# Kernel optimization log

Measured on AMD Instinct MI355X. Metric: run time of the kernel, lower is better.

Reference implementation:

```python
import jax, jax.numpy as jnp
import numpy as np

DT = 0.1    # arg.DELTA_T
BOX = 1.0   # arg.WORLD_SIZE
B = 8388608


def range_angle(ang):
    # wrap angle to [-pi, pi)
    return jnp.mod(ang + np.pi, 2.0 * np.pi) - np.pi


def setup_inputs() -> dict:
    key = jax.random.key(0)
    k1, k2, k3, k4, k5, k6 = jax.random.split(key, 6)
    x = jax.random.normal(k1, (B, 5), dtype=jnp.float32)          # [px,py,ang,vel,ang_vel]
    a = jax.random.uniform(k2, (B, 2), dtype=jnp.float32)          # actions [a_v, a_w]
    noise = jax.random.normal(k3, (B, 2), dtype=jnp.float32)       # standard-normal process noise
    pro_gains = jax.random.uniform(k4, (2,), dtype=jnp.float32)    # process gains
    pro_noise_ln_vars = jax.random.normal(k5, (2,), dtype=jnp.float32)  # log-variances
    goal_radius = jax.random.uniform(k6, (1,), dtype=jnp.float32)
    return {"x": x, "a": a, "noise": noise, "pro_gains": pro_gains,
            "pro_noise_ln_vars": pro_noise_ln_vars, "goal_radius": goal_radius}


def reference(x, a, noise, pro_gains, pro_noise_ln_vars, goal_radius):
    px, py, ang = x[:, 0], x[:, 1], x[:, 2]
    # w = sqrt(exp(ln_var)) * randn(2)  (noise pre-sampled, deterministic)
    std = jnp.sqrt(jnp.exp(pro_noise_ln_vars))            # [2]
    w = std * noise                                        # [B,2]
    vel = pro_gains[0] * a[:, 0] + w[:, 0]                 # 0*vel drops old vel
    ang_vel = pro_gains[1] * a[:, 1] + w[:, 1]
    ang = range_angle(ang + ang_vel * DT)
    px = jnp.clip(px + vel * jnp.cos(ang) * DT, -BOX, BOX)
    py = jnp.clip(py + vel * jnp.sin(ang) * DT, -BOX, BOX)
    next_x = jnp.stack([px, py, ang, vel, ang_vel], axis=-1)   # [B,5]
    reached_target = jnp.sqrt(px * px + py * py) <= goal_radius[0]  # [B] bool
    return next_x, reached_target
```

## Files before the change

kernel.cpp:

```cpp
#include <hip/hip_runtime.h>
#include <math.h>


__device__ __forceinline__ void step_one(
    float px0, float py0, float ang0,
    float ax, float ay, float n0, float n1,
    float g0, float g1, float std0, float std1, float gr,
    float& px, float& py, float& ang, float& vel, float& ang_vel, float& reach)
{
    const float DT    = 0.1f;
    const float PI_F  = 3.14159265358979323846f;
    const float TWOPI = 6.283185307179586f;

    const float w0 = __fmul_rn(std0, n0);
    const float w1 = __fmul_rn(std1, n1);
    vel     = __fadd_rn(__fmul_rn(g0, ax), w0);
    ang_vel = __fadd_rn(__fmul_rn(g1, ay), w1);

    const float t  = __fadd_rn(ang0, __fmul_rn(ang_vel, DT));
    const float tp = __fadd_rn(t, PI_F);
    float m = fmodf(tp, TWOPI);
    if (m < 0.0f) m = __fadd_rn(m, TWOPI);
    ang = __fsub_rn(m, PI_F);

    float s, c;
    sincosf(ang, &s, &c);

    px = __fadd_rn(px0, __fmul_rn(__fmul_rn(vel, c), DT));
    px = fminf(fmaxf(px, -1.0f), 1.0f);
    py = __fadd_rn(py0, __fmul_rn(__fmul_rn(vel, s), DT));
    py = fminf(fmaxf(py, -1.0f), 1.0f);

    const float r2 = __fadd_rn(__fmul_rn(px, px), __fmul_rn(py, py));
    const float r  = __fsqrt_rn(r2);
    reach = (r <= gr) ? 1.0f : 0.0f;
}

__global__ __launch_bounds__(256) void step_kernel(
    const float* __restrict__ x,
    const float* __restrict__ a,
    const float* __restrict__ noise,
    const float* __restrict__ pro_gains,
    const float* __restrict__ pro_noise_ln_vars,
    const float* __restrict__ goal_radius,
    float* __restrict__ out_next,
    float* __restrict__ out_reach,
    int n)
{
    const int nq = n >> 2;
    const int t = blockIdx.x * blockDim.x + threadIdx.x;

    const float g0   = pro_gains[0];
    const float g1   = pro_gains[1];
    const float std0 = __fsqrt_rn(expf(pro_noise_ln_vars[0]));
    const float std1 = __fsqrt_rn(expf(pro_noise_ln_vars[1]));
    const float gr   = goal_radius[0];

    if (t < nq) {
        const size_t st = (size_t)t;

        const float4* __restrict__ xq = (const float4*)x;
        const float4 q0 = xq[5 * st + 0];
        const float4 q1 = xq[5 * st + 1];
        const float4 q2 = xq[5 * st + 2];
        const float4 q3 = xq[5 * st + 3];
        const float4 q4 = xq[5 * st + 4];

        const float4* __restrict__ aq = (const float4*)a;
        const float4 av0 = aq[2 * st + 0];
        const float4 av1 = aq[2 * st + 1];
        const float4* __restrict__ nqv = (const float4*)noise;
        const float4 nv0 = nqv[2 * st + 0];
        const float4 nv1 = nqv[2 * st + 1];

        const float ipx[4]  = { q0.x, q1.y, q2.z, q3.w };
        const float ipy[4]  = { q0.y, q1.z, q2.w, q4.x };
        const float iang[4] = { q0.z, q1.w, q3.x, q4.y };
        const float iax[4]  = { av0.x, av0.z, av1.x, av1.z };
        const float iay[4]  = { av0.y, av0.w, av1.y, av1.w };
        const float in0[4]  = { nv0.x, nv0.z, nv1.x, nv1.z };
        const float in1[4]  = { nv0.y, nv0.w, nv1.y, nv1.w };

        float opx[4], opy[4], oang[4], ovel[4], oavl[4], orch[4];
#pragma unroll
        for (int k = 0; k < 4; ++k) {
            step_one(ipx[k], ipy[k], iang[k], iax[k], iay[k], in0[k], in1[k],
                     g0, g1, std0, std1, gr,
                     opx[k], opy[k], oang[k], ovel[k], oavl[k], orch[k]);
        }

        float4* __restrict__ oq = (float4*)out_next;
        oq[5 * st + 0] = make_float4(opx[0], opy[0], oang[0], ovel[0]);
        oq[5 * st + 1] = make_float4(oavl[0], opx[1], opy[1], oang[1]);
        oq[5 * st + 2] = make_float4(ovel[1], oavl[1], opx[2], opy[2]);
        oq[5 * st + 3] = make_float4(oang[2], ovel[2], oavl[2], opx[3]);
        oq[5 * st + 4] = make_float4(opy[3], oang[3], ovel[3], oavl[3]);
        ((float4*)out_reach)[st] = make_float4(orch[0], orch[1], orch[2], orch[3]);
    }

    if ((n & 3) && t == 0) {
        for (int i = nq * 4; i < n; ++i) {
            const size_t si = (size_t)i;
            float px, py, ang, vel, avl, rch;
            step_one(x[5 * si + 0], x[5 * si + 1], x[5 * si + 2],
                     a[2 * si + 0], a[2 * si + 1],
                     noise[2 * si + 0], noise[2 * si + 1],
                     g0, g1, std0, std1, gr, px, py, ang, vel, avl, rch);
            out_next[5 * si + 0] = px;
            out_next[5 * si + 1] = py;
            out_next[5 * si + 2] = ang;
            out_next[5 * si + 3] = vel;
            out_next[5 * si + 4] = avl;
            out_reach[si] = rch;
        }
    }
}

extern "C" void kernel_launch(void* const* d_in, const int* in_sizes, int n_in,
                              void* d_out, int out_size, void* d_ws, size_t ws_size,
                              hipStream_t stream) {
    const float* x       = (const float*)d_in[0];
    const float* a       = (const float*)d_in[1];
    const float* noise   = (const float*)d_in[2];
    const float* gains   = (const float*)d_in[3];
    const float* lnvars  = (const float*)d_in[4];
    const float* gradius = (const float*)d_in[5];

    const int n = in_sizes[0] / 5;
    float* out_next  = (float*)d_out;
    float* out_reach = (float*)d_out + (size_t)n * 5;

    const int nq = n >> 2;
    const int block = 256;
    int grid = (nq + block - 1) / block;
    if (grid < 1) grid = 1;
    step_kernel<<<grid, block, 0, stream>>>(x, a, noise, gains, lnvars, gradius,
                                            out_next, out_reach, n);
}
```

Before: 410.8 us.

## Stage rows through shared memory for coalesced float4 loads and stores

```diff
diff --git a/kernel.cpp b/kernel.cpp
--- a/kernel.cpp
+++ b/kernel.cpp
@@ -47,8 +47,8 @@
     float* __restrict__ out_reach,
     int n)
 {
-    const int nq = n >> 2;
-    const int t = blockIdx.x * blockDim.x + threadIdx.x;
+    const int t = threadIdx.x;
+    const long long rowbase = (long long)blockIdx.x * 256;
 
     const float g0   = pro_gains[0];
     const float g1   = pro_gains[1];
@@ -56,55 +56,62 @@
     const float std1 = __fsqrt_rn(expf(pro_noise_ln_vars[1]));
     const float gr   = goal_radius[0];
 
-    if (t < nq) {
-        const size_t st = (size_t)t;
+    __shared__ float4 sx4[320];
+    __shared__ float4 sa4[128];
+    __shared__ float4 sn4[128];
+    __shared__ float4 so4[320];
+    __shared__ float4 sr4[64];
 
-        const float4* __restrict__ xq = (const float4*)x;
-        const float4 q0 = xq[5 * st + 0];
-        const float4 q1 = xq[5 * st + 1];
-        const float4 q2 = xq[5 * st + 2];
-        const float4 q3 = xq[5 * st + 3];
-        const float4 q4 = xq[5 * st + 4];
+    if (rowbase + 256 <= (long long)n) {
+        const float4* __restrict__ xg = (const float4*)x + (size_t)blockIdx.x * 320;
+        sx4[t] = xg[t];
+        if (t < 64) sx4[256 + t] = xg[256 + t];
+        const float4* __restrict__ ag = (const float4*)a + (size_t)blockIdx.x * 128;
+        const float4* __restrict__ ng = (const float4*)noise + (size_t)blockIdx.x * 128;
+        if (t < 128) {
+            sa4[t] = ag[t];
+            sn4[t] = ng[t];
+        }
+        __syncthreads();
 
-        const float4* __restrict__ aq = (const float4*)a;
-        const float4 av0 = aq[2 * st + 0];
-        const float4 av1 = aq[2 * st + 1];
-        const float4* __restrict__ nqv = (const float4*)noise;
-        const float4 nv0 = nqv[2 * st + 0];
-        const float4 nv1 = nqv[2 * st + 1];
+        const float* sx = (const float*)sx4;
+        const float* sa = (const float*)sa4;
+        const float* sn = (const float*)sn4;
+        const float px0  = sx[5 * t + 0];
+        const float py0  = sx[5 * t + 1];
+        const float ang0 = sx[5 * t + 2];
+        const float ax   = sa[2 * t + 0];
+        const float ay   = sa[2 * t + 1];
+        const float n0   = sn[2 * t + 0];
+        const float n1   = sn[2 * t + 1];
 
-        const float ipx[4]  = { q0.x, q1.y, q2.z, q3.w };
-        const float ipy[4]  = { q0.y, q1.z, q2.w, q4.x };
-        const float iang[4] = { q0.z, q1.w, q3.x, q4.y };
-        const float iax[4]  = { av0.x, av0.z, av1.x, av1.z };
-        const float iay[4]  = { av0.y, av0.w, av1.y, av1.w };
-        const float in0[4]  = { nv0.x, nv0.z, nv1.x, nv1.z };
-        const float in1[4]  = { nv0.y, nv0.w, nv1.y, nv1.w };
+        float px, py, ang, vel, avl, rch;
+        step_one(px0, py0, ang0, ax, ay, n0, n1,
+                 g0, g1, std0, std1, gr, px, py, ang, vel, avl, rch);
 
-        float opx[4], opy[4], oang[4], ovel[4], oavl[4], orch[4];
-#pragma unroll
-        for (int k = 0; k < 4; ++k) {
-            step_one(ipx[k], ipy[k], iang[k], iax[k], iay[k], in0[k], in1[k],
-                     g0, g1, std0, std1, gr,
-                     opx[k], opy[k], oang[k], ovel[k], oavl[k], orch[k]);
-        }
+        float* so = (float*)so4;
+        so[5 * t + 0] = px;
+        so[5 * t + 1] = py;
+        so[5 * t + 2] = ang;
+        so[5 * t + 3] = vel;
+        so[5 * t + 4] = avl;
+        ((float*)sr4)[t] = rch;
+        __syncthreads();
 
-        float4* __restrict__ oq = (float4*)out_next;
-        oq[5 * st + 0] = make_float4(opx[0], opy[0], oang[0], ovel[0]);
-        oq[5 * st + 1] = make_float4(oavl[0], opx[1], opy[1], oang[1]);
-        oq[5 * st + 2] = make_float4(ovel[1], oavl[1], opx[2], opy[2]);
-        oq[5 * st + 3] = make_float4(oang[2], ovel[2], oavl[2], opx[3]);
-        oq[5 * st + 4] = make_float4(opy[3], oang[3], ovel[3], oavl[3]);
-        ((float4*)out_reach)[st] = make_float4(orch[0], orch[1], orch[2], orch[3]);
-    }
-
-    if ((n & 3) && t == 0) {
-        for (int i = nq * 4; i < n; ++i) {
+        float4* __restrict__ og = (float4*)out_next + (size_t)blockIdx.x * 320;
+        og[t] = so4[t];
+        if (t < 64) og[256 + t] = so4[256 + t];
+        float4* __restrict__ rg = (float4*)out_reach + (size_t)blockIdx.x * 64;
+        if (t < 64) rg[t] = sr4[t];
+    } else {
+        const long long i = rowbase + t;
+        if (i < (long long)n) {
             const size_t si = (size_t)i;
+            const float2 av = *(const float2*)(a + 2 * si);
+            const float2 nv = *(const float2*)(noise + 2 * si);
             float px, py, ang, vel, avl, rch;
             step_one(x[5 * si + 0], x[5 * si + 1], x[5 * si + 2],
-                     a[2 * si + 0], a[2 * si + 1],
-                     noise[2 * si + 0], noise[2 * si + 1],
+                     av.x, av.y, nv.x, nv.y,
                      g0, g1, std0, std1, gr, px, py, ang, vel, avl, rch);
             out_next[5 * si + 0] = px;
             out_next[5 * si + 1] = py;
@@ -130,10 +137,8 @@
     float* out_next  = (float*)d_out;
     float* out_reach = (float*)d_out + (size_t)n * 5;
 
-    const int nq = n >> 2;
     const int block = 256;
-    int grid = (nq + block - 1) / block;
-    if (grid < 1) grid = 1;
+    const int grid = (int)(((long long)n + 255) / 256);
     step_kernel<<<grid, block, 0, stream>>>(x, a, noise, gains, lnvars, gradius,
                                             out_next, out_reach, n);
 }
```

New measurement: 389.1 us. 5.3% less time.
